# Performance work log

Measured on AMD Instinct MI355X. Metric: run time of the kernel, lower is better.

The kernel has to match this reference:

```python
import jax, jax.numpy as jnp
import numpy as np

B, S, D = 2, 2048, 4096
NH, NKV = 32, 8
HD = D // NH          # 128
NREP = NH // NKV      # 4
THETA = 10000.0


def _rope_tables(seq_len, head_dim):
    inv = 1.0 / (THETA ** (jnp.arange(0, head_dim, 2, dtype=jnp.float32) / head_dim))  # [HD/2]
    t = jnp.arange(seq_len, dtype=jnp.float32)
    ang = jnp.outer(t, inv)                      # [S, HD/2]
    return jnp.cos(ang), jnp.sin(ang)


def _apply_rope(x, cos, sin):
    # x: [b, s, h, d]; interleaved pairs (even=real, odd=imag), matching view_as_complex
    xr = x.reshape(*x.shape[:-1], HD // 2, 2)
    x0, x1 = xr[..., 0], xr[..., 1]
    c = cos[None, :, None, :]
    s = sin[None, :, None, :]
    o0 = x0 * c - x1 * s
    o1 = x0 * s + x1 * c
    return jnp.stack([o0, o1], axis=-1).reshape(x.shape)


def setup_inputs() -> dict:
    key = jax.random.key(0)
    ks = jax.random.split(key, 5)
    sc = 0.02
    return {
        "x": jax.random.normal(ks[0], (B, S, D), jnp.float32),
        "wq": jax.random.normal(ks[1], (D, NH * HD), jnp.float32) * sc,
        "wk": jax.random.normal(ks[2], (D, NKV * HD), jnp.float32) * sc,
        "wv": jax.random.normal(ks[3], (D, NKV * HD), jnp.float32) * sc,
        "wo": jax.random.normal(ks[4], (NH * HD, D), jnp.float32) * sc,
        "start_pos": 0,
        "inference": 0,
    }


def reference(x, wq, wk, wv, wo, start_pos, inference):
    bsz, seq_len, _ = x.shape
    # QKV projections (training path: inference=False)
    xq = (x @ wq).reshape(bsz, seq_len, NH, HD)
    xk = (x @ wk).reshape(bsz, seq_len, NKV, HD)
    xv = (x @ wv).reshape(bsz, seq_len, NKV, HD)

    cos, sin = _rope_tables(seq_len, HD)
    xq = _apply_rope(xq, cos, sin)
    xk = _apply_rope(xk, cos, sin)

    # GQA without materializing repeated KV: group q heads per kv head
    q = xq.reshape(bsz, seq_len, NKV, NREP, HD)           # [b, s, g, r, d]
    scores = jnp.einsum('bqgrd,bkgd->bgrqk', q, xk) / np.sqrt(HD)
    causal = jnp.triu(jnp.full((seq_len, seq_len), -jnp.inf, jnp.float32), k=1)
    scores = scores + causal
    probs = jax.nn.softmax(scores.astype(jnp.float32), axis=-1).astype(x.dtype)
    out = jnp.einsum('bgrqk,bkgd->bqgrd', probs, xv)      # [b, s, g, r, d]
    out = out.reshape(bsz, seq_len, NH * HD)
    return out @ wo
```

## Files before the change

### kernel.cpp

```cpp
#include <hip/hip_runtime.h>
#include <hip/hip_bf16.h>

#define B_ 2
#define S_ 2048
#define D_ 4096
#define NH_ 32
#define NKV_ 8
#define HD_ 128
#define NREP_ 4

typedef unsigned short u16;
typedef __attribute__((ext_vector_type(8))) short short8;
typedef __attribute__((ext_vector_type(4))) float f32x4;

__device__ inline float bf2f(u16 u) {
    union { unsigned u; float f; } v; v.u = ((unsigned)u) << 16; return v.f;
}
__device__ inline u16 f2bf(float f) {
    union { float f; unsigned u; } v; v.f = f;
    unsigned r = v.u + 0x7fffu + ((v.u >> 16) & 1u);
    return (u16)(r >> 16);
}
__device__ inline unsigned pack_bf16(float a, float b) {
    return (unsigned)f2bf(a) | ((unsigned)f2bf(b) << 16);
}

__device__ inline void gl_lds16(const u16* g, u16* l) {
    __builtin_amdgcn_global_load_lds(
        (const __attribute__((address_space(1))) unsigned int*)g,
        (__attribute__((address_space(3))) unsigned int*)l, 16, 0, 0);
}

__global__ __launch_bounds__(256) void conv_k(const float* __restrict__ in,
                                              u16* __restrict__ out) {
    size_t i = ((size_t)blockIdx.x * 256 + threadIdx.x) * 4;
    float4 v = *(const float4*)&in[i];
    u16 t[4] = {f2bf(v.x), f2bf(v.y), f2bf(v.z), f2bf(v.w)};
    *(uint2*)&out[i] = *(const uint2*)t;
}

__global__ __launch_bounds__(256) void tconv_k(const float* __restrict__ in,
                                               u16* __restrict__ out,
                                               int R, int C) {
    __shared__ u16 tile[64][65];
    int bx = blockIdx.x * 64, by = blockIdx.y * 64;
    int tx = threadIdx.x, ty = threadIdx.y;
    for (int i = ty; i < 64; i += 4)
        tile[i][tx] = f2bf(in[(size_t)(by + i) * C + bx + tx]);
    __syncthreads();
    for (int i = ty; i < 64; i += 4)
        out[(size_t)(bx + i) * R + by + tx] = tile[tx][i];
}

__global__ __launch_bounds__(256) void transpose_k(const u16* __restrict__ in,
                                                   u16* __restrict__ out,
                                                   int R, int C) {
    __shared__ u16 tile[64][65];
    int bx = blockIdx.x * 64, by = blockIdx.y * 64;
    int tx = threadIdx.x, ty = threadIdx.y;
    for (int i = ty; i < 64; i += 4)
        tile[i][tx] = in[(size_t)(by + i) * C + bx + tx];
    __syncthreads();
    for (int i = ty; i < 64; i += 4)
        out[(size_t)(bx + i) * R + by + tx] = tile[tx][i];
}

template <int OUT_F32>
__global__ __launch_bounds__(256) void gemm_bt(const u16* __restrict__ A,
                                               const u16* __restrict__ Bt,
                                               void* __restrict__ Cv,
                                               int M, int N, int K) {
    __shared__ __align__(16) u16 As[128 * 32];
    __shared__ __align__(16) u16 Bs[128 * 32];
    int tid = threadIdx.x;
    int w = tid >> 6, lane = tid & 63;
    int ln = lane & 15, qd = lane >> 4;
    int wr = w >> 1, wc = w & 1;
    int m0 = blockIdx.y * 128, n0 = blockIdx.x * 128;

    int srow = lane >> 2;
    int skk  = (lane & 3) * 8;
    const u16* Ag = A  + (size_t)(m0 + w * 32 + srow) * K + skk;
    const u16* Bg = Bt + (size_t)(n0 + w * 32 + srow) * K + skk;

    f32x4 acc[4][4];
#pragma unroll
    for (int i = 0; i < 4; ++i)
#pragma unroll
        for (int j = 0; j < 4; ++j)
            acc[i][j] = f32x4{0.f, 0.f, 0.f, 0.f};

    for (int k0 = 0; k0 < K; k0 += 32) {
#pragma unroll
        for (int t = 0; t < 2; ++t) {
            gl_lds16(Ag + (size_t)(t * 16) * K + k0, &As[(w * 32 + t * 16) * 32]);
            gl_lds16(Bg + (size_t)(t * 16) * K + k0, &Bs[(w * 32 + t * 16) * 32]);
        }
        __syncthreads();
        short8 af[4], bfr[4];
#pragma unroll
        for (int i = 0; i < 4; ++i)
            af[i] = *(const short8*)&As[(wr * 64 + i * 16 + ln) * 32 + qd * 8];
#pragma unroll
        for (int j = 0; j < 4; ++j)
            bfr[j] = *(const short8*)&Bs[(wc * 64 + j * 16 + ln) * 32 + qd * 8];
#pragma unroll
        for (int i = 0; i < 4; ++i)
#pragma unroll
            for (int j = 0; j < 4; ++j)
                acc[i][j] = __builtin_amdgcn_mfma_f32_16x16x32_bf16(af[i], bfr[j], acc[i][j], 0, 0, 0);
        __syncthreads();
    }
#pragma unroll
    for (int i = 0; i < 4; ++i)
#pragma unroll
        for (int j = 0; j < 4; ++j)
#pragma unroll
            for (int r = 0; r < 4; ++r) {
                int row = m0 + wr * 64 + i * 16 + qd * 4 + r;
                int col = n0 + wc * 64 + j * 16 + ln;
                if (OUT_F32)
                    ((float*)Cv)[(size_t)row * N + col] = acc[i][j][r];
                else
                    ((u16*)Cv)[(size_t)row * N + col] = f2bf(acc[i][j][r]);
            }
}


__device__ inline short8 lds_frag(const u16* base, int row, int colb) {
    int lin = ((row & 127) << 7) + colb;
    int off = ((row >> 7) << 14) + (lin ^ (((lin >> 9) & 1) << 5));
    return *(const short8*)((const char*)base + off);
}

__device__ inline void stage_half(const u16* g, int row0, int ldK, int k0,
                                  u16* ldsHalf, int w, int lane) {
#pragma unroll
    for (int j = 0; j < 2; ++j) {
        int Lb = (w << 11) + (j << 10) + (lane << 4);
        int src = Lb ^ (((Lb >> 9) & 1) << 5);
        const u16* gp = g + (size_t)(row0 + (src >> 7)) * ldK + k0 + ((src & 127) >> 1);
        gl_lds16(gp, ldsHalf + (((w << 11) + (j << 10)) >> 1));
    }
}

#define PH_MFMA(MB)                                                           \
    asm volatile("s_waitcnt lgkmcnt(0)" ::: "memory");                        \
    __builtin_amdgcn_sched_barrier(0);                                        \
    __builtin_amdgcn_s_setprio(1);                                            \
    _Pragma("unroll") for (int mi = 0; mi < 2; ++mi)                          \
      _Pragma("unroll") for (int ni = 0; ni < 4; ++ni)                        \
        _Pragma("unroll") for (int kk = 0; kk < 2; ++kk)                      \
          acc[(MB) + mi][ni] = __builtin_amdgcn_mfma_f32_16x16x32_bf16(       \
              af[mi][kk], bfr[ni][kk], acc[(MB) + mi][ni], 0, 0, 0);          \
    __builtin_amdgcn_s_setprio(0);                                            \
    __builtin_amdgcn_s_barrier();

#define TILE_BODY(T, CURA, CURB, OTHA)                                        \
  {                                                                           \
    const int t_ = (T);                                                       \
    const bool p1_ = (t_ + 1 < nt), p2_ = (t_ + 2 < nt);                      \
    short8 bfr[4][2], af[2][2];                                               \
                       \
    _Pragma("unroll") for (int ni = 0; ni < 4; ++ni)                          \
      _Pragma("unroll") for (int kk = 0; kk < 2; ++kk)                        \
        bfr[ni][kk] = lds_frag(CURB, wn * 64 + ni * 16 + ln, kk * 64 + qd * 16); \
    _Pragma("unroll") for (int mi = 0; mi < 2; ++mi)                          \
      _Pragma("unroll") for (int kk = 0; kk < 2; ++kk)                        \
        af[mi][kk] = lds_frag(CURA, wm * 128 + mi * 16 + ln, kk * 64 + qd * 16); \
    if (p1_) stage_half(Ag, 0, K, (t_ + 1) << 6, OTHA, w, lane);              \
    asm volatile("s_waitcnt lgkmcnt(8)" ::: "memory");                        \
    __builtin_amdgcn_s_barrier();                                             \
    PH_MFMA(0)                                                                \
                                    \
    _Pragma("unroll") for (int mi = 0; mi < 2; ++mi)                          \
      _Pragma("unroll") for (int kk = 0; kk < 2; ++kk)                        \
        af[mi][kk] = lds_frag(CURA, wm * 128 + (mi + 2) * 16 + ln, kk * 64 + qd * 16); \
    if (p1_) stage_half(Ag, 128, K, (t_ + 1) << 6, OTHA + 8192, w, lane);     \
    __builtin_amdgcn_s_barrier();                                             \
    PH_MFMA(2)                                                                \
                                    \
    _Pragma("unroll") for (int mi = 0; mi < 2; ++mi)                          \
      _Pragma("unroll") for (int kk = 0; kk < 2; ++kk)                        \
        af[mi][kk] = lds_frag(CURA, wm * 128 + (mi + 4) * 16 + ln, kk * 64 + qd * 16); \
    if (p2_) stage_half(Bg, 0, K, (t_ + 2) << 6, CURB, w, lane);              \
    __builtin_amdgcn_s_barrier();                                             \
    PH_MFMA(4)                                                                \
                     \
    _Pragma("unroll") for (int mi = 0; mi < 2; ++mi)                          \
      _Pragma("unroll") for (int kk = 0; kk < 2; ++kk)                        \
        af[mi][kk] = lds_frag(CURA, wm * 128 + (mi + 6) * 16 + ln, kk * 64 + qd * 16); \
    if (p2_) {                                                                \
        stage_half(Bg, 128, K, (t_ + 2) << 6, CURB + 8192, w, lane);          \
        asm volatile("s_waitcnt vmcnt(4)" ::: "memory");                      \
    } else if (p1_) {                                                         \
        asm volatile("s_waitcnt vmcnt(0)" ::: "memory");                      \
    }                                                                         \
    __builtin_amdgcn_s_barrier();                                             \
    PH_MFMA(6)                                                                \
  }

template <int OUT_F32>
__global__ __launch_bounds__(512, 1) void gemm256(const u16* __restrict__ A,
                                                  const u16* __restrict__ Bt,
                                                  void* __restrict__ Cv,
                                                  int M, int N, int K) {
    __shared__ __align__(16) u16 As[2][16384];
    __shared__ __align__(16) u16 Bs[2][16384];

    int tid = threadIdx.x;
    int w = tid >> 6, lane = tid & 63;
    int ln = lane & 15, qd = lane >> 4;
    int wm = w >> 2, wn = w & 3;

    int nbx = N >> 8;
    int cpx = gridDim.x >> 3;
    int bid = blockIdx.x;
    int swz = (bid & 7) * cpx + (bid >> 3);
    int m0 = (swz / nbx) << 8;
    int n0 = (swz % nbx) << 8;

    const u16* Ag = A + (size_t)m0 * K;
    const u16* Bg = Bt + (size_t)n0 * K;
    int nt = K >> 6;

    f32x4 acc[8][4];
#pragma unroll
    for (int i = 0; i < 8; ++i)
#pragma unroll
        for (int j = 0; j < 4; ++j) acc[i][j] = f32x4{0.f, 0.f, 0.f, 0.f};

    u16* A0 = &As[0][0]; u16* A1v = &As[1][0];
    u16* B0 = &Bs[0][0]; u16* B1v = &Bs[1][0];

    stage_half(Ag, 0,   K, 0,  A0,         w, lane);
    stage_half(Ag, 128, K, 0,  A0 + 8192,  w, lane);
    stage_half(Bg, 0,   K, 0,  B0,         w, lane);
    stage_half(Bg, 128, K, 0,  B0 + 8192,  w, lane);
    stage_half(Bg, 0,   K, 64, B1v,        w, lane);
    stage_half(Bg, 128, K, 64, B1v + 8192, w, lane);
    asm volatile("s_waitcnt vmcnt(4)" ::: "memory");
    __builtin_amdgcn_s_barrier();

    for (int tt = 0; tt < nt; tt += 2) {
        TILE_BODY(tt,     A0,  B0,  A1v)
        TILE_BODY(tt + 1, A1v, B1v, A0)
    }

#pragma unroll
    for (int mi = 0; mi < 8; ++mi)
#pragma unroll
        for (int ni = 0; ni < 4; ++ni)
#pragma unroll
            for (int r = 0; r < 4; ++r) {
                int row = m0 + wm * 128 + mi * 16 + qd * 4 + r;
                int col = n0 + wn * 64 + ni * 16 + ln;
                if (OUT_F32)
                    ((float*)Cv)[(size_t)row * N + col] = acc[mi][ni][r];
                else
                    ((u16*)Cv)[(size_t)row * N + col] = f2bf(acc[mi][ni][r]);
            }
}

__global__ void rope_k(u16* __restrict__ buf, int nheads, float scale) {
    int total = B_ * S_ * nheads * (HD_ / 2);
    int i = blockIdx.x * blockDim.x + threadIdx.x;
    if (i >= total) return;
    int p = i & 63;
    int h = (i >> 6) % nheads;
    int row = i / (64 * nheads);
    int s = row & (S_ - 1);
    float freq = __expf(-(float)(2 * p) * (9.210340371976184f / 128.0f));
    float ang = (float)s * freq;
    float c, sn;
    sincosf(ang, &sn, &c);
    size_t base = ((size_t)row * nheads + h) * HD_ + 2 * p;
    float x0 = bf2f(buf[base]), x1 = bf2f(buf[base + 1]);
    buf[base]     = f2bf((x0 * c - x1 * sn) * scale);
    buf[base + 1] = f2bf((x0 * sn + x1 * c) * scale);
}

__global__ __launch_bounds__(512) void attn_k(const u16* __restrict__ Q,
                                              const u16* __restrict__ K,
                                              const u16* __restrict__ Vt,
                                              u16* __restrict__ AO) {
    __shared__ __align__(16) u16 Ks[2][64 * 136];
    __shared__ __align__(16) u16 Vts[2][128 * 72];

    int tid = threadIdx.x;
    int w = tid >> 6, lane = tid & 63;
    int ln = lane & 15, qd = lane >> 4;

    int h  = blockIdx.y;
    int b  = blockIdx.z;
    int g  = h >> 2;

    const u16* Kbase = K + (size_t)(b * S_) * (NKV_ * HD_) + g * HD_;
    const u16* Vtb   = Vt + ((size_t)(b * NKV_ + g)) * HD_ * S_;

    int kr0 = tid >> 4, kb0 = (tid & 15) * 8;
    int kr1 = (tid + 512) >> 4, kb1 = kb0;
    int vr0 = tid >> 3, vb0 = (tid & 7) * 8;
    int vr1 = (tid + 512) >> 3, vb1 = vb0;

    for (int pass = 0; pass < 2; ++pass) {
        int qt = pass ? (S_ / 128 - 1 - (int)blockIdx.x) : (int)blockIdx.x;
        int q0 = qt * 128;

        const u16* qptr = Q + ((size_t)(b * S_ + q0 + w * 16 + ln)) * (NH_ * HD_) + h * HD_;
        short8 bq[4];
#pragma unroll
        for (int kq = 0; kq < 4; ++kq)
            bq[kq] = *(const short8*)(qptr + kq * 32 + qd * 8);

        f32x4 ot[8];
#pragma unroll
        for (int db = 0; db < 8; ++db) ot[db] = f32x4{0.f, 0.f, 0.f, 0.f};
        float m_s = -1e30f, l_s = 0.f;

        int nk = 2 * qt + 2;
        int qg = q0 + w * 16 + ln;
        int qmaxw = q0 + w * 16 + 15;

        {
            int4 a0 = *(const int4*)(Kbase + (size_t)kr0 * (NKV_ * HD_) + kb0);
            int4 a1 = *(const int4*)(Kbase + (size_t)kr1 * (NKV_ * HD_) + kb1);
            int4 v0 = *(const int4*)(Vtb + (size_t)vr0 * S_ + vb0);
            int4 v1 = *(const int4*)(Vtb + (size_t)vr1 * S_ + vb1);
            *(int4*)&Ks[0][kr0 * 136 + kb0] = a0;
            *(int4*)&Ks[0][kr1 * 136 + kb1] = a1;
            *(int4*)&Vts[0][vr0 * 72 + vb0] = v0;
            *(int4*)&Vts[0][vr1 * 72 + vb1] = v1;
        }
        __syncthreads();

        for (int kt = 0; kt < nk; ++kt) {
            int bb = kt & 1;
            int k0 = kt * 64;
            bool pf = (kt + 1 < nk);
            int4 pa0, pa1, pv0, pv1;
            if (pf) {
                int k0n = k0 + 64;
                pa0 = *(const int4*)(Kbase + (size_t)(k0n + kr0) * (NKV_ * HD_) + kb0);
                pa1 = *(const int4*)(Kbase + (size_t)(k0n + kr1) * (NKV_ * HD_) + kb1);
                pv0 = *(const int4*)(Vtb + (size_t)vr0 * S_ + k0n + vb0);
                pv1 = *(const int4*)(Vtb + (size_t)vr1 * S_ + k0n + vb1);
            }

            if (k0 <= qmaxw) {
                f32x4 st[4];
#pragma unroll
                for (int kb = 0; kb < 4; ++kb) st[kb] = f32x4{0.f, 0.f, 0.f, 0.f};
#pragma unroll
                for (int kb = 0; kb < 4; ++kb)
#pragma unroll
                    for (int kq = 0; kq < 4; ++kq) {
                        short8 ak = *(const short8*)&Ks[bb][(kb * 16 + ln) * 136 + kq * 32 + qd * 8];
                        st[kb] = __builtin_amdgcn_mfma_f32_16x16x32_bf16(ak, bq[kq], st[kb], 0, 0, 0);
                    }
                float mx = -1e30f;
#pragma unroll
                for (int kb = 0; kb < 4; ++kb)
#pragma unroll
                    for (int r = 0; r < 4; ++r) {
                        int kg = k0 + kb * 16 + qd * 4 + r;
                        if (kg > qg) st[kb][r] = -1e30f;
                        mx = fmaxf(mx, st[kb][r]);
                    }
                mx = fmaxf(mx, __shfl_xor(mx, 16, 64));
                mx = fmaxf(mx, __shfl_xor(mx, 32, 64));
                float mn = fmaxf(m_s, mx);
                float alpha = __expf(m_s - mn);
                m_s = mn;
                float rs = 0.f;
#pragma unroll
                for (int kb = 0; kb < 4; ++kb)
#pragma unroll
                    for (int r = 0; r < 4; ++r) {
                        float pv = __expf(st[kb][r] - mn);
                        st[kb][r] = pv;
                        rs += pv;
                    }
                rs += __shfl_xor(rs, 16, 64);
                rs += __shfl_xor(rs, 32, 64);
                l_s = l_s * alpha + rs;
#pragma unroll
                for (int db = 0; db < 8; ++db)
#pragma unroll
                    for (int r = 0; r < 4; ++r) ot[db][r] *= alpha;

                unsigned pk[4][2];
#pragma unroll
                for (int kb = 0; kb < 4; ++kb) {
                    pk[kb][0] = pack_bf16(st[kb][0], st[kb][1]);
                    pk[kb][1] = pack_bf16(st[kb][2], st[kb][3]);
                }
                int sA = ((qd & 1) << 5) + ln;
                int sB = sA + 16;
                bool hi = (qd & 2) != 0;
#pragma unroll
                for (int ks = 0; ks < 2; ++ks) {
                    unsigned t0a = (unsigned)__shfl((int)pk[2 * ks][0], sA, 64);
                    unsigned t0b = (unsigned)__shfl((int)pk[2 * ks][1], sA, 64);
                    unsigned t1a = (unsigned)__shfl((int)pk[2 * ks + 1][0], sA, 64);
                    unsigned t1b = (unsigned)__shfl((int)pk[2 * ks + 1][1], sA, 64);
                    unsigned t2a = (unsigned)__shfl((int)pk[2 * ks][0], sB, 64);
                    unsigned t2b = (unsigned)__shfl((int)pk[2 * ks][1], sB, 64);
                    unsigned t3a = (unsigned)__shfl((int)pk[2 * ks + 1][0], sB, 64);
                    unsigned t3b = (unsigned)__shfl((int)pk[2 * ks + 1][1], sB, 64);
                    union { unsigned u[4]; short8 s8; } bp;
                    bp.u[0] = hi ? t1a : t0a;
                    bp.u[1] = hi ? t1b : t0b;
                    bp.u[2] = hi ? t3a : t2a;
                    bp.u[3] = hi ? t3b : t2b;
#pragma unroll
                    for (int db = 0; db < 8; ++db) {
                        short8 av = *(const short8*)&Vts[bb][(db * 16 + ln) * 72 + ks * 32 + qd * 8];
                        ot[db] = __builtin_amdgcn_mfma_f32_16x16x32_bf16(av, bp.s8, ot[db], 0, 0, 0);
                    }
                }
            }

            if (pf) {
                int nb = bb ^ 1;
                *(int4*)&Ks[nb][kr0 * 136 + kb0] = pa0;
                *(int4*)&Ks[nb][kr1 * 136 + kb1] = pa1;
                *(int4*)&Vts[nb][vr0 * 72 + vb0] = pv0;
                *(int4*)&Vts[nb][vr1 * 72 + vb1] = pv1;
            }
            __syncthreads();
        }

        float invl = 1.0f / l_s;
        size_t orow = (size_t)(b * S_ + q0 + w * 16 + ln) * (NH_ * HD_) + h * HD_;
#pragma unroll
        for (int db = 0; db < 8; ++db) {
            u16 t[4];
#pragma unroll
            for (int r = 0; r < 4; ++r) t[r] = f2bf(ot[db][r] * invl);
            *(uint2*)&AO[orow + db * 16 + qd * 4] = *(const uint2*)t;
        }
    }
}

extern "C" void kernel_launch(void* const* d_in, const int* in_sizes, int n_in,
                              void* d_out, int out_size, void* d_ws, size_t ws_size,
                              hipStream_t stream) {
    const float* x  = (const float*)d_in[0];
    const float* wq = (const float*)d_in[1];
    const float* wk = (const float*)d_in[2];
    const float* wv = (const float*)d_in[3];
    const float* wo = (const float*)d_in[4];
    float* out = (float*)d_out;

    char* p = (char*)d_ws;
    auto alloc = [&](size_t nelem) { u16* r = (u16*)p; p += nelem * 2; return r; };
    u16* xb  = alloc(4096ull * 4096);
    u16* wqT = alloc(4096ull * 4096);
    u16* wkT = alloc(1024ull * 4096);
    u16* wvT = alloc(1024ull * 4096);
    u16* Q   = alloc(4096ull * 4096);
    u16* Kb  = alloc(4096ull * 1024);
    u16* Vb  = alloc(4096ull * 1024);
    u16* AO  = alloc(4096ull * 4096);

    dim3 tblk(64, 4);
    conv_k<<<16384, 256, 0, stream>>>(x, xb);
    tconv_k<<<dim3(64, 64), tblk, 0, stream>>>(wq, wqT, 4096, 4096);
    tconv_k<<<dim3(16, 64), tblk, 0, stream>>>(wk, wkT, 4096, 1024);
    tconv_k<<<dim3(16, 64), tblk, 0, stream>>>(wv, wvT, 4096, 1024);

    gemm256<0><<<256, 512, 0, stream>>>(xb, wqT, Q, 4096, 4096, 4096);
    gemm_bt<0><<<dim3(8, 32), 256, 0, stream>>>(xb, wkT, Kb, 4096, 1024, 4096);
    gemm_bt<0><<<dim3(8, 32), 256, 0, stream>>>(xb, wvT, Vb, 4096, 1024, 4096);

    u16* woT = xb;
    u16* Vt  = wqT;
    tconv_k<<<dim3(64, 64), tblk, 0, stream>>>(wo, woT, 4096, 4096);

    int totq = B_ * S_ * NH_ * (HD_ / 2);
    rope_k<<<(totq + 255) / 256, 256, 0, stream>>>(Q, NH_, 0.08838834764831845f);
    int totk = B_ * S_ * NKV_ * (HD_ / 2);
    rope_k<<<(totk + 255) / 256, 256, 0, stream>>>(Kb, NKV_, 1.0f);

    for (int b = 0; b < B_; ++b)
        transpose_k<<<dim3(16, 32), tblk, 0, stream>>>(
            Vb + (size_t)b * S_ * (NKV_ * HD_), Vt + (size_t)b * (NKV_ * HD_) * S_, S_, NKV_ * HD_);

    attn_k<<<dim3(S_ / 256, NH_, B_), 512, 0, stream>>>(Q, Kb, Vt, AO);

    gemm256<1><<<256, 512, 0, stream>>>(AO, woT, out, 4096, 4096, 4096);
}
```

Baseline: 879.5 us.

## Merge small launches, vectorize RoPE, and streamline attention softmax with exp2 and lazy rescale

Merges the K/V weight conversions, the K/V projection GEMMs, the Q/K RoPE passes and the per-batch V transposes into single launches, and vectorizes RoPE to eight elements per thread. Float-to-bf16 packing now uses the hardware pack-convert instruction instead of manual rounding. The attention softmax folds log2(e) into the Q scale so it can use raw exp2. It skips rescaling the running output unless the max grows by more than a threshold. The causal mask is applied only on diagonal tiles, and MFMA sections get raised wave priority. This cuts launch overhead and VALU work in attention, at the cost of slightly looser numerics from the lazy rescale and the approximate exp.

Result: faster. 756.2 us (-14.0%).

```diff
diff --git a/kernel.cpp b/kernel.cpp
--- a/kernel.cpp
+++ b/kernel.cpp
@@ -21,8 +21,15 @@
     unsigned r = v.u + 0x7fffu + ((v.u >> 16) & 1u);
     return (u16)(r >> 16);
 }
-__device__ inline unsigned pack_bf16(float a, float b) {
-    return (unsigned)f2bf(a) | ((unsigned)f2bf(b) << 16);
+__device__ inline unsigned cvt_pk(float lo, float hi) {
+    unsigned r;
+    asm("v_cvt_pk_bf16_f32 %0, %1, %2" : "=v"(r) : "v"(lo), "v"(hi));
+    return r;
+}
+__device__ inline float exp2_fast(float x) {
+    float r;
+    asm("v_exp_f32 %0, %1" : "=v"(r) : "v"(x));
+    return r;
 }
 
 __device__ inline void gl_lds16(const u16* g, u16* l) {
@@ -35,8 +42,10 @@
                                               u16* __restrict__ out) {
     size_t i = ((size_t)blockIdx.x * 256 + threadIdx.x) * 4;
     float4 v = *(const float4*)&in[i];
-    u16 t[4] = {f2bf(v.x), f2bf(v.y), f2bf(v.z), f2bf(v.w)};
-    *(uint2*)&out[i] = *(const uint2*)t;
+    uint2 t;
+    t.x = cvt_pk(v.x, v.y);
+    t.y = cvt_pk(v.z, v.w);
+    *(uint2*)&out[i] = t;
 }
 
 __global__ __launch_bounds__(256) void tconv_k(const float* __restrict__ in,
@@ -52,24 +61,43 @@
         out[(size_t)(bx + i) * R + by + tx] = tile[tx][i];
 }
 
+__global__ __launch_bounds__(256) void tconv2_k(const float* __restrict__ in0,
+                                                const float* __restrict__ in1,
+                                                u16* __restrict__ out0,
+                                                u16* __restrict__ out1,
+                                                int R, int C) {
+    __shared__ u16 tile[64][65];
+    const float* in = blockIdx.z ? in1 : in0;
+    u16* out = blockIdx.z ? out1 : out0;
+    int bx = blockIdx.x * 64, by = blockIdx.y * 64;
+    int tx = threadIdx.x, ty = threadIdx.y;
+    for (int i = ty; i < 64; i += 4)
+        tile[i][tx] = f2bf(in[(size_t)(by + i) * C + bx + tx]);
+    __syncthreads();
+    for (int i = ty; i < 64; i += 4)
+        out[(size_t)(bx + i) * R + by + tx] = tile[tx][i];
+}
+
 __global__ __launch_bounds__(256) void transpose_k(const u16* __restrict__ in,
                                                    u16* __restrict__ out,
                                                    int R, int C) {
     __shared__ u16 tile[64][65];
+    const u16* ib = in + (size_t)blockIdx.z * R * C;
+    u16* ob = out + (size_t)blockIdx.z * R * C;
     int bx = blockIdx.x * 64, by = blockIdx.y * 64;
     int tx = threadIdx.x, ty = threadIdx.y;
     for (int i = ty; i < 64; i += 4)
-        tile[i][tx] = in[(size_t)(by + i) * C + bx + tx];
+        tile[i][tx] = ib[(size_t)(by + i) * C + bx + tx];
     __syncthreads();
     for (int i = ty; i < 64; i += 4)
-        out[(size_t)(bx + i) * R + by + tx] = tile[tx][i];
-}
-
-template <int OUT_F32>
-__global__ __launch_bounds__(256) void gemm_bt(const u16* __restrict__ A,
+        ob[(size_t)(bx + i) * R + by + tx] = tile[tx][i];
+}
+
+__global__ __launch_bounds__(256) void gemm_kv(const u16* __restrict__ A,
                                                const u16* __restrict__ Bt,
-                                               void* __restrict__ Cv,
-                                               int M, int N, int K) {
+                                               u16* __restrict__ Kout,
+                                               u16* __restrict__ Vout,
+                                               int M, int K) {
     __shared__ __align__(16) u16 As[128 * 32];
     __shared__ __align__(16) u16 Bs[128 * 32];
     int tid = threadIdx.x;
@@ -111,6 +139,8 @@
                 acc[i][j] = __builtin_amdgcn_mfma_f32_16x16x32_bf16(af[i], bfr[j], acc[i][j], 0, 0, 0);
         __syncthreads();
     }
+    u16* dst = (n0 < 1024) ? Kout : Vout;
+    int nb = (n0 < 1024) ? n0 : (n0 - 1024);
 #pragma unroll
     for (int i = 0; i < 4; ++i)
 #pragma unroll
@@ -118,14 +148,10 @@
 #pragma unroll
             for (int r = 0; r < 4; ++r) {
                 int row = m0 + wr * 64 + i * 16 + qd * 4 + r;
-                int col = n0 + wc * 64 + j * 16 + ln;
-                if (OUT_F32)
-                    ((float*)Cv)[(size_t)row * N + col] = acc[i][j][r];
-                else
-                    ((u16*)Cv)[(size_t)row * N + col] = f2bf(acc[i][j][r]);
+                int col = nb + wc * 64 + j * 16 + ln;
+                dst[(size_t)row * 1024 + col] = f2bf(acc[i][j][r]);
             }
 }
-
 
 __device__ inline short8 lds_frag(const u16* base, int row, int colb) {
     int lin = ((row & 127) << 7) + colb;
@@ -161,7 +187,6 @@
     const int t_ = (T);                                                       \
     const bool p1_ = (t_ + 1 < nt), p2_ = (t_ + 2 < nt);                      \
     short8 bfr[4][2], af[2][2];                                               \
-                       \
     _Pragma("unroll") for (int ni = 0; ni < 4; ++ni)                          \
       _Pragma("unroll") for (int kk = 0; kk < 2; ++kk)                        \
         bfr[ni][kk] = lds_frag(CURB, wn * 64 + ni * 16 + ln, kk * 64 + qd * 16); \
@@ -172,21 +197,18 @@
     asm volatile("s_waitcnt lgkmcnt(8)" ::: "memory");                        \
     __builtin_amdgcn_s_barrier();                                             \
     PH_MFMA(0)                                                                \
-                                    \
     _Pragma("unroll") for (int mi = 0; mi < 2; ++mi)                          \
       _Pragma("unroll") for (int kk = 0; kk < 2; ++kk)                        \
         af[mi][kk] = lds_frag(CURA, wm * 128 + (mi + 2) * 16 + ln, kk * 64 + qd * 16); \
     if (p1_) stage_half(Ag, 128, K, (t_ + 1) << 6, OTHA + 8192, w, lane);     \
     __builtin_amdgcn_s_barrier();                                             \
     PH_MFMA(2)                                                                \
-                                    \
     _Pragma("unroll") for (int mi = 0; mi < 2; ++mi)                          \
       _Pragma("unroll") for (int kk = 0; kk < 2; ++kk)                        \
         af[mi][kk] = lds_frag(CURA, wm * 128 + (mi + 4) * 16 + ln, kk * 64 + qd * 16); \
     if (p2_) stage_half(Bg, 0, K, (t_ + 2) << 6, CURB, w, lane);              \
     __builtin_amdgcn_s_barrier();                                             \
     PH_MFMA(4)                                                                \
-                     \
     _Pragma("unroll") for (int mi = 0; mi < 2; ++mi)                          \
       _Pragma("unroll") for (int kk = 0; kk < 2; ++kk)                        \
         af[mi][kk] = lds_frag(CURA, wm * 128 + (mi + 6) * 16 + ln, kk * 64 + qd * 16); \
@@ -262,22 +284,38 @@
             }
 }
 
-__global__ void rope_k(u16* __restrict__ buf, int nheads, float scale) {
-    int total = B_ * S_ * nheads * (HD_ / 2);
-    int i = blockIdx.x * blockDim.x + threadIdx.x;
-    if (i >= total) return;
-    int p = i & 63;
-    int h = (i >> 6) % nheads;
-    int row = i / (64 * nheads);
+__global__ __launch_bounds__(256) void rope_k(u16* __restrict__ Q,
+                                              u16* __restrict__ Kb,
+                                              float qscale) {
+    const int ngq = B_ * S_ * NH_ * (HD_ / 8);
+    const int ngk = B_ * S_ * NKV_ * (HD_ / 8);
+    int i = blockIdx.x * 256 + threadIdx.x;
+    u16* buf; int nheads; float scale;
+    if (i < ngq) { buf = Q; nheads = NH_; scale = qscale; }
+    else {
+        i -= ngq;
+        if (i >= ngk) return;
+        buf = Kb; nheads = NKV_; scale = 1.f;
+    }
+    int gp = i & 15;
+    int hh = (i >> 4) % nheads;
+    int row = i / (16 * nheads);
     int s = row & (S_ - 1);
-    float freq = __expf(-(float)(2 * p) * (9.210340371976184f / 128.0f));
-    float ang = (float)s * freq;
-    float c, sn;
-    sincosf(ang, &sn, &c);
-    size_t base = ((size_t)row * nheads + h) * HD_ + 2 * p;
-    float x0 = bf2f(buf[base]), x1 = bf2f(buf[base + 1]);
-    buf[base]     = f2bf((x0 * c - x1 * sn) * scale);
-    buf[base + 1] = f2bf((x0 * sn + x1 * c) * scale);
+    size_t base = ((size_t)row * nheads + hh) * HD_ + gp * 8;
+    uint4 v = *(const uint4*)&buf[base];
+    unsigned ov[4];
+    unsigned* vp = (unsigned*)&v;
+#pragma unroll
+    for (int j = 0; j < 4; ++j) {
+        int p = gp * 4 + j;
+        float freq = __expf(-(float)(2 * p) * (9.210340371976184f / 128.0f));
+        float ang = (float)s * freq;
+        float c, sn;
+        sincosf(ang, &sn, &c);
+        float x0 = bf2f((u16)vp[j]), x1 = bf2f((u16)(vp[j] >> 16));
+        ov[j] = cvt_pk((x0 * c - x1 * sn) * scale, (x0 * sn + x1 * c) * scale);
+    }
+    *(uint4*)&buf[base] = *(uint4*)ov;
 }
 
 __global__ __launch_bounds__(512) void attn_k(const u16* __restrict__ Q,
@@ -306,8 +344,12 @@
     for (int pass = 0; pass < 2; ++pass) {
         int qt = pass ? (S_ / 128 - 1 - (int)blockIdx.x) : (int)blockIdx.x;
         int q0 = qt * 128;
-
-        const u16* qptr = Q + ((size_t)(b * S_ + q0 + w * 16 + ln)) * (NH_ * HD_) + h * HD_;
+        int qb = q0 + w * 16;
+        int qg = qb + ln;
+        int ntw   = ((qb + 15) >> 6) + 1;
+        int nfull = (qb + 1) >> 6;
+
+        const u16* qptr = Q + ((size_t)(b * S_ + qg)) * (NH_ * HD_) + h * HD_;
         short8 bq[4];
 #pragma unroll
         for (int kq = 0; kq < 4; ++kq)
@@ -319,8 +361,6 @@
         float m_s = -1e30f, l_s = 0.f;
 
         int nk = 2 * qt + 2;
-        int qg = q0 + w * 16 + ln;
-        int qmaxw = q0 + w * 16 + 15;
 
         {
             int4 a0 = *(const int4*)(Kbase + (size_t)kr0 * (NKV_ * HD_) + kb0);
@@ -347,10 +387,11 @@
                 pv1 = *(const int4*)(Vtb + (size_t)vr1 * S_ + k0n + vb1);
             }
 
-            if (k0 <= qmaxw) {
+            if (kt < ntw) {
                 f32x4 st[4];
 #pragma unroll
                 for (int kb = 0; kb < 4; ++kb) st[kb] = f32x4{0.f, 0.f, 0.f, 0.f};
+                __builtin_amdgcn_s_setprio(1);
 #pragma unroll
                 for (int kb = 0; kb < 4; ++kb)
 #pragma unroll
@@ -358,42 +399,58 @@
                         short8 ak = *(const short8*)&Ks[bb][(kb * 16 + ln) * 136 + kq * 32 + qd * 8];
                         st[kb] = __builtin_amdgcn_mfma_f32_16x16x32_bf16(ak, bq[kq], st[kb], 0, 0, 0);
                     }
-                float mx = -1e30f;
-#pragma unroll
-                for (int kb = 0; kb < 4; ++kb)
-#pragma unroll
-                    for (int r = 0; r < 4; ++r) {
-                        int kg = k0 + kb * 16 + qd * 4 + r;
-                        if (kg > qg) st[kb][r] = -1e30f;
-                        mx = fmaxf(mx, st[kb][r]);
-                    }
+                __builtin_amdgcn_s_setprio(0);
+
+                float mx;
+                if (kt >= nfull) {
+                    int lim = qg - k0 - qd * 4;
+                    mx = -1e30f;
+#pragma unroll
+                    for (int kb = 0; kb < 4; ++kb)
+#pragma unroll
+                        for (int r = 0; r < 4; ++r) {
+                            if (16 * kb + r > lim) st[kb][r] = -1e30f;
+                            mx = fmaxf(mx, st[kb][r]);
+                        }
+                } else {
+                    mx = st[0][0];
+#pragma unroll
+                    for (int kb = 0; kb < 4; ++kb)
+#pragma unroll
+                        for (int r = 0; r < 4; ++r)
+                            if (kb + r) mx = fmaxf(mx, st[kb][r]);
+                }
                 mx = fmaxf(mx, __shfl_xor(mx, 16, 64));
                 mx = fmaxf(mx, __shfl_xor(mx, 32, 64));
-                float mn = fmaxf(m_s, mx);
-                float alpha = __expf(m_s - mn);
-                m_s = mn;
+
+                if (__any(mx > m_s + 8.f)) {
+                    float mn = fmaxf(m_s, mx);
+                    float alpha = exp2_fast(m_s - mn);
+                    m_s = mn;
+                    l_s *= alpha;
+#pragma unroll
+                    for (int db = 0; db < 8; ++db)
+#pragma unroll
+                        for (int r = 0; r < 4; ++r) ot[db][r] *= alpha;
+                }
                 float rs = 0.f;
 #pragma unroll
                 for (int kb = 0; kb < 4; ++kb)
 #pragma unroll
                     for (int r = 0; r < 4; ++r) {
-                        float pv = __expf(st[kb][r] - mn);
+                        float pv = exp2_fast(st[kb][r] - m_s);
                         st[kb][r] = pv;
                         rs += pv;
                     }
                 rs += __shfl_xor(rs, 16, 64);
                 rs += __shfl_xor(rs, 32, 64);
-                l_s = l_s * alpha + rs;
-#pragma unroll
-                for (int db = 0; db < 8; ++db)
-#pragma unroll
-                    for (int r = 0; r < 4; ++r) ot[db][r] *= alpha;
+                l_s += rs;
 
                 unsigned pk[4][2];
 #pragma unroll
                 for (int kb = 0; kb < 4; ++kb) {
-                    pk[kb][0] = pack_bf16(st[kb][0], st[kb][1]);
-                    pk[kb][1] = pack_bf16(st[kb][2], st[kb][3]);
+                    pk[kb][0] = cvt_pk(st[kb][0], st[kb][1]);
+                    pk[kb][1] = cvt_pk(st[kb][2], st[kb][3]);
                 }
                 int sA = ((qd & 1) << 5) + ln;
                 int sB = sA + 16;
@@ -413,32 +470,34 @@
                     bp.u[1] = hi ? t1b : t0b;
                     bp.u[2] = hi ? t3a : t2a;
                     bp.u[3] = hi ? t3b : t2b;
+                    __builtin_amdgcn_s_setprio(1);
 #pragma unroll
                     for (int db = 0; db < 8; ++db) {
                         short8 av = *(const short8*)&Vts[bb][(db * 16 + ln) * 72 + ks * 32 + qd * 8];
                         ot[db] = __builtin_amdgcn_mfma_f32_16x16x32_bf16(av, bp.s8, ot[db], 0, 0, 0);
                     }
+                    __builtin_amdgcn_s_setprio(0);
                 }
             }
 
             if (pf) {
-                int nb = bb ^ 1;
-                *(int4*)&Ks[nb][kr0 * 136 + kb0] = pa0;
-                *(int4*)&Ks[nb][kr1 * 136 + kb1] = pa1;
-                *(int4*)&Vts[nb][vr0 * 72 + vb0] = pv0;
-                *(int4*)&Vts[nb][vr1 * 72 + vb1] = pv1;
+                int nb2 = bb ^ 1;
+                *(int4*)&Ks[nb2][kr0 * 136 + kb0] = pa0;
+                *(int4*)&Ks[nb2][kr1 * 136 + kb1] = pa1;
+                *(int4*)&Vts[nb2][vr0 * 72 + vb0] = pv0;
+                *(int4*)&Vts[nb2][vr1 * 72 + vb1] = pv1;
             }
             __syncthreads();
         }
 
         float invl = 1.0f / l_s;
-        size_t orow = (size_t)(b * S_ + q0 + w * 16 + ln) * (NH_ * HD_) + h * HD_;
+        size_t orow = (size_t)(b * S_ + qg) * (NH_ * HD_) + h * HD_;
 #pragma unroll
         for (int db = 0; db < 8; ++db) {
-            u16 t[4];
-#pragma unroll
-            for (int r = 0; r < 4; ++r) t[r] = f2bf(ot[db][r] * invl);
-            *(uint2*)&AO[orow + db * 16 + qd * 4] = *(const uint2*)t;
+            uint2 t2;
+            t2.x = cvt_pk(ot[db][0] * invl, ot[db][1] * invl);
+            t2.y = cvt_pk(ot[db][2] * invl, ot[db][3] * invl);
+            *(uint2*)&AO[orow + db * 16 + qd * 4] = t2;
         }
     }
 }
@@ -467,25 +526,19 @@
     dim3 tblk(64, 4);
     conv_k<<<16384, 256, 0, stream>>>(x, xb);
     tconv_k<<<dim3(64, 64), tblk, 0, stream>>>(wq, wqT, 4096, 4096);
-    tconv_k<<<dim3(16, 64), tblk, 0, stream>>>(wk, wkT, 4096, 1024);
-    tconv_k<<<dim3(16, 64), tblk, 0, stream>>>(wv, wvT, 4096, 1024);
+    tconv2_k<<<dim3(16, 64, 2), tblk, 0, stream>>>(wk, wv, wkT, wvT, 4096, 1024);
 
     gemm256<0><<<256, 512, 0, stream>>>(xb, wqT, Q, 4096, 4096, 4096);
-    gemm_bt<0><<<dim3(8, 32), 256, 0, stream>>>(xb, wkT, Kb, 4096, 1024, 4096);
-    gemm_bt<0><<<dim3(8, 32), 256, 0, stream>>>(xb, wvT, Vb, 4096, 1024, 4096);
+    gemm_kv<<<dim3(16, 32), 256, 0, stream>>>(xb, wkT, Kb, Vb, 4096, 4096);
 
     u16* woT = xb;
     u16* Vt  = wqT;
     tconv_k<<<dim3(64, 64), tblk, 0, stream>>>(wo, woT, 4096, 4096);
 
-    int totq = B_ * S_ * NH_ * (HD_ / 2);
-    rope_k<<<(totq + 255) / 256, 256, 0, stream>>>(Q, NH_, 0.08838834764831845f);
-    int totk = B_ * S_ * NKV_ * (HD_ / 2);
-    rope_k<<<(totk + 255) / 256, 256, 0, stream>>>(Kb, NKV_, 1.0f);
-
-    for (int b = 0; b < B_; ++b)
-        transpose_k<<<dim3(16, 32), tblk, 0, stream>>>(
-            Vb + (size_t)b * S_ * (NKV_ * HD_), Vt + (size_t)b * (NKV_ * HD_) * S_, S_, NKV_ * HD_);
+    int ng = B_ * S_ * NH_ * (HD_ / 8) + B_ * S_ * NKV_ * (HD_ / 8);
+    rope_k<<<(ng + 255) / 256, 256, 0, stream>>>(Q, Kb, 0.12751743f);
+
+    transpose_k<<<dim3(16, 32, 2), tblk, 0, stream>>>(Vb, Vt, S_, NKV_ * HD_);
 
     attn_k<<<dim3(S_ / 256, NH_, B_), 512, 0, stream>>>(Q, Kb, Vt, AO);
 
```
